# Optimization experiments

Measured on AMD Instinct MI355X. Metric: run time of the kernel, lower is better.

## Reference

```python
import jax, jax.numpy as jnp
import numpy as np

ALPHA = 0.2
NEG_INF = -9e15


def setup_inputs() -> dict:
    key = jax.random.key(0)
    k1, k2, k3, k4 = jax.random.split(key, 4)
    B, N, C_IN, C_OUT, R, H = 8, 1024, 256, 256, 4, 4
    node_feats = jax.random.normal(k1, (B, N, C_IN), dtype=jnp.float32)
    adj_matrix = jax.random.randint(k2, (B, N, N, R), 0, 2, dtype=jnp.int32)
    # xavier_uniform with gain=1.414 for Linear(c_in, c_out) weights
    lim_w = 1.414 * np.sqrt(6.0 / (C_IN + C_OUT))
    W = jax.random.uniform(k3, (R, C_IN, C_OUT), minval=-lim_w, maxval=lim_w, dtype=jnp.float32)
    c_per = C_OUT // H
    lim_a = 1.414 * np.sqrt(6.0 / (H + 2 * c_per))
    a = jax.random.uniform(k4, (R, H, 2 * c_per), minval=-lim_a, maxval=lim_a, dtype=jnp.float32)
    return {"node_feats": node_feats, "adj_matrix": adj_matrix, "W": W, "a": a}


def reference(node_feats, adj_matrix, W, a):
    B, N, _ = node_feats.shape
    R, H = a.shape[0], a.shape[1]
    C = a.shape[2] // 2  # per-head feature dim
    out = jnp.zeros((B, N, H, C), dtype=node_feats.dtype)
    for r in range(R):
        # per-relation projection: [B,N,H,C]
        f = jnp.einsum('bnc,cd->bnd', node_feats, W[r]).reshape(B, N, H, C)
        a_l, a_r = a[r, :, :C], a[r, :, C:]
        # attention logit decomposes: a . [f_i || f_j] = a_l . f_i + a_r . f_j
        li = jnp.einsum('bnhc,hc->bnh', f, a_l)  # source-node term
        lj = jnp.einsum('bnhc,hc->bnh', f, a_r)  # target-node term
        logits = jax.nn.leaky_relu(li[:, :, None, :] + lj[:, None, :, :], ALPHA)  # [B,N,N,H]
        mask = adj_matrix[..., r] != 0  # [B,N,N]
        logits = jnp.where(mask[..., None], logits, NEG_INF)
        probs = jax.nn.softmax(logits, axis=2)
        out = out + jnp.einsum('bijh,bjhc->bihc', probs, f)
    # concat_heads=True
    return out.reshape(B, N, H * C)
```

## Files before the change

### kernel.cpp

```cpp
#include <hip/hip_runtime.h>
#include <math.h>

#define Bsz 8
#define Nn 1024
#define CIN 256
#define COUT 256
#define NR 4
#define NH 4

typedef unsigned short u16;
typedef __attribute__((ext_vector_type(8))) short bf16x8;
typedef __attribute__((ext_vector_type(4))) float f32x4;
typedef __attribute__((ext_vector_type(2))) float f32x2;

#define OFF_LIP (16u << 20)
#define OFF_LJP ((16u << 20) + (512u << 10))
#define OFF_ADJM (17u << 20)
#define OFF_XBF (21u << 20)
#define OFF_WBFT (25u << 20)
#define OFF_WAL ((25u << 20) + (512u << 10))
#define OFF_WAR ((25u << 20) + (528u << 10))
#define OFF_OUTR (26u << 20)

#define LOG2E 1.4426950408889634f

__device__ __forceinline__ short f2bf(float x) {
  union { float f; unsigned u; } v; v.f = x;
  unsigned r = (v.u + 0x7FFFu + ((v.u >> 16) & 1u)) >> 16;
  return (short)r;
}

__device__ __forceinline__ float fast_exp2(float x) {
#if __has_builtin(__builtin_amdgcn_exp2f)
  return __builtin_amdgcn_exp2f(x);
#else
  return exp2f(x);
#endif
}

__device__ __forceinline__ int sbfe1(unsigned v, int bit) {
#if __has_builtin(__builtin_amdgcn_sbfe)
  return __builtin_amdgcn_sbfe((int)v, bit, 1);
#else
  return ((int)(v << (31 - bit))) >> 31;
#endif
}

__device__ __forceinline__ unsigned perm_hi16(unsigned hi, unsigned lo) {
#if __has_builtin(__builtin_amdgcn_perm)
  return __builtin_amdgcn_perm(hi, lo, 0x07060302u);
#else
  return (lo >> 16) | (hi & 0xFFFF0000u);
#endif
}

__device__ __forceinline__ void gl_lds16(const void* g, void* l) {
  __builtin_amdgcn_global_load_lds(
      (const __attribute__((address_space(1))) unsigned int*)(unsigned long long)g,
      (__attribute__((address_space(3))) unsigned int*)(unsigned int)(unsigned long long)l,
      16, 0, 0);
}

__global__ __launch_bounds__(256, 8)
void gatt_pack(const int4* __restrict__ adj4, unsigned long long* __restrict__ adjm) {
  const int t = threadIdx.x;
  const int wid = blockIdx.x * 4 + (t >> 6);
  const int lane = t & 63;
  const int jw = wid & 15;
  const int i = (wid >> 4) & 1023;
  const int b = wid >> 14;
  const int j = jw * 64 + lane;
  const int4 av = adj4[(size_t)(b * Nn + i) * Nn + j];
  const unsigned long long b0 = __ballot(av.x != 0);
  const unsigned long long b1 = __ballot(av.y != 0);
  const unsigned long long b2 = __ballot(av.z != 0);
  const unsigned long long b3 = __ballot(av.w != 0);
  if (lane < 4) {
    unsigned long long v = (lane == 0) ? b0 : (lane == 1) ? b1 : (lane == 2) ? b2 : b3;
    adjm[((size_t)((b * Nn + i) * NR + lane)) * 16 + jw] = v;
  }
}

__global__ __launch_bounds__(256, 4)
void gatt_prep(const float* __restrict__ W, const float* __restrict__ a,
               u16* __restrict__ WbfT, float* __restrict__ wa_l,
               float* __restrict__ wa_r) {
  const int t = threadIdx.x;
  if (blockIdx.x < 32) {
    const int r = blockIdx.x >> 3, kc = blockIdx.x & 7;
    u16 pk[32];
#pragma unroll 8
    for (int kk = 0; kk < 32; ++kk)
      pk[kk] = (u16)f2bf(W[(size_t)r * 65536 + (size_t)(kc * 32 + kk) * COUT + t]);
    u16* dst = WbfT + (size_t)r * 65536 + (size_t)t * CIN + kc * 32;
#pragma unroll
    for (int q = 0; q < 4; ++q) *(int4*)(dst + q * 8) = *(int4*)(pk + q * 8);
  } else {
    const int cb = blockIdx.x - 32;
    const int r = cb >> 2, h = cb & 3;
    float sl = 0.f, sr = 0.f;
    const float* Wp = W + (size_t)r * 65536 + (size_t)t * COUT + h * 64;
    const float* ap = a + r * 512 + h * 128;
#pragma unroll 8
    for (int c = 0; c < 64; ++c) {
      const float wv = Wp[c];
      sl = fmaf(wv, ap[c], sl);
      sr = fmaf(wv, ap[64 + c], sr);
    }
    wa_l[(size_t)cb * CIN + t] = sl;
    wa_r[(size_t)cb * CIN + t] = sr;
  }
}

__global__ __launch_bounds__(256, 4)
void gatt_logitx(const float* __restrict__ X, const float4* __restrict__ wal4,
                 const float4* __restrict__ war4, float* __restrict__ Lip,
                 float* __restrict__ Ljp, u16* __restrict__ Xbf) {
  __shared__ float Xs[16 * 260];
  const int t = threadIdx.x;
  const int row0 = blockIdx.x * 16;
  {
    const int il = t >> 4, kq = t & 15;
    const float4* xp = (const float4*)(X + (size_t)(row0 + il) * CIN + kq * 16);
    float4 v[4];
    u16 pk[16];
#pragma unroll
    for (int u = 0; u < 4; ++u) {
      v[u] = xp[u];
      pk[u * 4 + 0] = (u16)f2bf(v[u].x);
      pk[u * 4 + 1] = (u16)f2bf(v[u].y);
      pk[u * 4 + 2] = (u16)f2bf(v[u].z);
      pk[u * 4 + 3] = (u16)f2bf(v[u].w);
    }
    float4* dst = (float4*)(Xs + il * 260 + kq * 16);
#pragma unroll
    for (int u = 0; u < 4; ++u) dst[u] = v[u];
    u16* xb = Xbf + (size_t)(row0 + il) * CIN + kq * 16;
    *(int4*)xb = *(int4*)pk;
    *(int4*)(xb + 8) = *(int4*)(pk + 8);
  }
  __syncthreads();
  const int rl = t >> 4, combo = t & 15;
  float li = 0.f, lj = 0.f;
#pragma unroll 8
  for (int k4 = 0; k4 < 64; ++k4) {
    const float4 x4 = *(const float4*)(Xs + rl * 260 + k4 * 4);
    const float4 wl = wal4[combo * 64 + k4];
    const float4 wr = war4[combo * 64 + k4];
    li += x4.x * wl.x + x4.y * wl.y + x4.z * wl.z + x4.w * wl.w;
    lj += x4.x * wr.x + x4.y * wr.y + x4.z * wr.z + x4.w * wr.w;
  }
  const int g = row0 + rl, b = g >> 10, n = g & 1023;
  const size_t idx = ((size_t)(combo * Bsz + b)) * Nn + n;
  Lip[idx] = li * LOG2E;
  Ljp[idx] = lj * LOG2E;
}

__global__ __launch_bounds__(256)
void gatt_fgemm(const u16* __restrict__ Xbf, const u16* __restrict__ WbfT,
                u16* __restrict__ fTf) {
  __shared__ u16 lds_w[8192];
  __shared__ u16 lds_x[2048];
  const int t = threadIdx.x;
  const int r = blockIdx.x & 3, b = (blockIdx.x >> 2) & 7, ntl = blockIdx.x >> 5;
  const int n0 = ntl * 64;
  const int g0 = b * Nn + n0;
  const int lane = t & 63, w = t >> 6;
  const int m = lane & 15, quad = lane >> 4;
  const int cw = w * 64;
  const int xq = quad ^ (m & 3);

  const u16* Wsrc = WbfT + (size_t)r * 65536;
  f32x4 acc[4][4];
#pragma unroll
  for (int ct = 0; ct < 4; ++ct)
#pragma unroll
    for (int nt = 0; nt < 4; ++nt) acc[ct][nt] = (f32x4){0.f, 0.f, 0.f, 0.f};

  for (int kc = 0; kc < 8; ++kc) {
    __syncthreads();
#pragma unroll
    for (int q = 0; q < 4; ++q) {
      const int s = q * 256 + t;
      const int c = s >> 2, ks = (s & 3) ^ (c & 3);
      gl_lds16(Wsrc + (size_t)c * CIN + kc * 32 + ks * 8, lds_w + s * 8);
    }
    {
      const int s = t;
      const int n = s >> 2, ks = (s & 3) ^ (n & 3);
      gl_lds16(Xbf + (size_t)(g0 + n) * CIN + kc * 32 + ks * 8, lds_x + s * 8);
    }
    __syncthreads();

    bf16x8 af[4], bfr[4];
#pragma unroll
    for (int ct = 0; ct < 4; ++ct)
      af[ct] = *(const bf16x8*)(lds_w + (cw + ct * 16 + m) * 32 + xq * 8);
#pragma unroll
    for (int nt = 0; nt < 4; ++nt)
      bfr[nt] = *(const bf16x8*)(lds_x + (nt * 16 + m) * 32 + xq * 8);
#pragma unroll
    for (int ct = 0; ct < 4; ++ct)
#pragma unroll
      for (int nt = 0; nt < 4; ++nt)
        acc[ct][nt] = __builtin_amdgcn_mfma_f32_16x16x32_bf16(af[ct], bfr[nt], acc[ct][nt], 0, 0, 0);
  }

  u16* fragbase = fTf + (size_t)(((r * Bsz + b) * 4 + w) * 128) * 512;
#pragma unroll
  for (int ct = 0; ct < 4; ++ct) {
#pragma unroll
    for (int ntf = 0; ntf < 4; ++ntf) {
      const int j = n0 + ntf * 16 + m;
      const int jb = j >> 5;
      const int qt = ((ntf & 1) << 1) | (m >> 3);
      const int e = m & 7;
      u16* dst = fragbase + (size_t)((jb * 4 + ct) * 512) + (qt * 16 + quad * 4) * 8 + e;
#pragma unroll
      for (int p = 0; p < 4; ++p) dst[p * 8] = (u16)f2bf(acc[ct][ntf][p]);
    }
  }
}

__global__ __launch_bounds__(256, 4)
void gatt_attn(const unsigned long long* __restrict__ adjm,
               const u16* __restrict__ fTf, const float* __restrict__ Lip,
               const float* __restrict__ Ljp, float* __restrict__ outr) {
  __shared__ float ljs[4 * 1024];

  const int t = threadIdx.x;
  const int comb = blockIdx.x & 31;
  const int b = comb >> 2, r = comb & 3;
  const int i0 = (blockIdx.x >> 5) * 32;
  const int h = t >> 6, lane = t & 63;
  const int m = lane & 15, quad = lane >> 4;
  const int qo = quad * 8;

  {
#pragma unroll
    for (int q = 0; q < 4; ++q) {
      const int s = q * 256 + t;
      const int hh = s >> 8, off = s & 255;
      ((float4*)ljs)[hh * 256 + off] =
          ((const float4*)(Ljp + ((size_t)((r * NH + hh) * Bsz + b)) * Nn))[off];
    }
  }
  __syncthreads();

  const float* lipb = Lip + ((size_t)((r * NH + h) * Bsz + b)) * Nn;
  const float li0 = lipb[i0 + m];
  const float li1 = lipb[i0 + 16 + m];
  const unsigned long long* amp0 = adjm + ((size_t)((b * Nn + i0 + m) * NR + r)) * 16;
  const unsigned long long* amp1 = adjm + ((size_t)((b * Nn + i0 + 16 + m) * NR + r)) * 16;
  const bf16x8* fp = (const bf16x8*)fTf + (size_t)(((r * Bsz + b) * 4 + h)) * 8192;
  const float* ljh = ljs + h * Nn;

  bf16x8 ones;
#pragma unroll
  for (int e = 0; e < 8; ++e) ones[e] = (short)0x3F80;

  f32x4 acc[2][4], den[2];
#pragma unroll
  for (int iw = 0; iw < 2; ++iw) {
    den[iw] = (f32x4){0.f, 0.f, 0.f, 0.f};
#pragma unroll
    for (int nt = 0; nt < 4; ++nt) acc[iw][nt] = (f32x4){0.f, 0.f, 0.f, 0.f};
  }

  for (int jq = 0; jq < 16; ++jq) {
    const uint2 mw0 = *(const uint2*)(amp0 + jq);
    const uint2 mw1 = *(const uint2*)(amp1 + jq);
#pragma unroll
    for (int half = 0; half < 2; ++half) {
      const int jb = jq * 2 + half;
      const unsigned w0 = half ? mw0.y : mw0.x;
      const unsigned w1 = half ? mw1.y : mw1.x;
      const f32x2* lj2p = (const f32x2*)(ljh + jb * 32 + qo);
      bf16x8 bfr[4];
#pragma unroll
      for (int nt = 0; nt < 4; ++nt) bfr[nt] = fp[(jb * 4 + nt) * 64 + lane];
#pragma unroll
      for (int iw = 0; iw < 2; ++iw) {
        const float liv = iw ? li1 : li0;
        const unsigned mb = (iw ? w1 : w0) >> qo;
        const f32x2 li2 = {liv, liv};
        unsigned afu[4];
#pragma unroll
        for (int pr = 0; pr < 4; ++pr) {
          const f32x2 s2 = li2 + lj2p[pr];
          const f32x2 s02 = s2 * 0.2f;
          const float t0 = fmaxf(s2.x, s02.x);
          const float t1 = fmaxf(s2.y, s02.y);
          const unsigned e0 =
              __float_as_uint(fast_exp2(t0)) & (unsigned)sbfe1(mb, 2 * pr);
          const unsigned e1 =
              __float_as_uint(fast_exp2(t1)) & (unsigned)sbfe1(mb, 2 * pr + 1);
          afu[pr] = perm_hi16(e1, e0);
        }
        union { unsigned u[4]; bf16x8 v; } af;
        af.u[0] = afu[0]; af.u[1] = afu[1]; af.u[2] = afu[2]; af.u[3] = afu[3];
        den[iw] = __builtin_amdgcn_mfma_f32_16x16x32_bf16(af.v, ones, den[iw], 0, 0, 0);
#pragma unroll
        for (int nt = 0; nt < 4; ++nt)
          acc[iw][nt] = __builtin_amdgcn_mfma_f32_16x16x32_bf16(af.v, bfr[nt], acc[iw][nt], 0, 0, 0);
      }
    }
  }

#pragma unroll
  for (int iw = 0; iw < 2; ++iw) {
#pragma unroll
    for (int p = 0; p < 4; ++p) {
      const float inv = __builtin_amdgcn_rcpf(den[iw][p]);
      const int i = i0 + iw * 16 + quad * 4 + p;
      float* op = outr + (((size_t)(r * Bsz + b) * Nn) + i) * COUT + h * 64 + m;
#pragma unroll
      for (int nt = 0; nt < 4; ++nt) op[nt * 16] = acc[iw][nt][p] * inv;
    }
  }
}

__global__ __launch_bounds__(256, 8)
void gatt_reduce(const float4* __restrict__ outr4, float4* __restrict__ out4) {
  const int idx = blockIdx.x * 256 + threadIdx.x;
  float4 v0 = outr4[idx];
  float4 v1 = outr4[idx + 524288];
  float4 v2 = outr4[idx + 2 * 524288];
  float4 v3 = outr4[idx + 3 * 524288];
  out4[idx] = make_float4(v0.x + v1.x + v2.x + v3.x, v0.y + v1.y + v2.y + v3.y,
                          v0.z + v1.z + v2.z + v3.z, v0.w + v1.w + v2.w + v3.w);
}

extern "C" void kernel_launch(void* const* d_in, const int* in_sizes, int n_in,
                              void* d_out, int out_size, void* d_ws, size_t ws_size,
                              hipStream_t stream) {
  const float* X = (const float*)d_in[0];
  const int4* adj4 = (const int4*)d_in[1];
  const float* W = (const float*)d_in[2];
  const float* a = (const float*)d_in[3];
  float* out = (float*)d_out;

  char* ws = (char*)d_ws;
  u16* fTf = (u16*)ws;
  float* Lip = (float*)(ws + OFF_LIP);
  float* Ljp = (float*)(ws + OFF_LJP);
  unsigned long long* adjm = (unsigned long long*)(ws + OFF_ADJM);
  u16* Xbf = (u16*)(ws + OFF_XBF);
  u16* WbfT = (u16*)(ws + OFF_WBFT);
  float* wa_l = (float*)(ws + OFF_WAL);
  float* wa_r = (float*)(ws + OFF_WAR);
  float* outr = (float*)(ws + OFF_OUTR);

  gatt_pack<<<dim3(32768), dim3(256), 0, stream>>>(adj4, adjm);
  gatt_prep<<<dim3(48), dim3(256), 0, stream>>>(W, a, WbfT, wa_l, wa_r);
  gatt_logitx<<<dim3(512), dim3(256), 0, stream>>>(X, (const float4*)wa_l,
                                                   (const float4*)wa_r, Lip, Ljp, Xbf);
  gatt_fgemm<<<dim3(512), dim3(256), 0, stream>>>(Xbf, WbfT, fTf);
  gatt_attn<<<dim3(1024), dim3(256), 0, stream>>>(adjm, fTf, Lip, Ljp, outr);
  gatt_reduce<<<dim3(2048), dim3(256), 0, stream>>>((const float4*)outr, (float4*)out);
}
```

Measured before the change: 295.2 us.

## Fuse relation reduction into attention kernel via shared-memory accumulation

The attention kernel now uses 1024-thread blocks, so all four relations and four heads of a 32-row tile run in one block. Per-relation outputs are summed in shared memory in turn, with barriers between relations, and written straight to the final output. This removes the 32 MB intermediate buffer round trip and the separate reduce launch. The cost is a 4x smaller grid (256 blocks) with larger blocks, more shared memory (64 KB), and serialized accumulation steps that may cut occupancy and latency hiding.

```diff
diff --git a/kernel.cpp b/kernel.cpp
--- a/kernel.cpp
+++ b/kernel.cpp
@@ -20,7 +20,6 @@
 #define OFF_WBFT (25u << 20)
 #define OFF_WAL ((25u << 20) + (512u << 10))
 #define OFF_WAR ((25u << 20) + (528u << 10))
-#define OFF_OUTR (26u << 20)
 
 #define LOG2E 1.4426950408889634f
 
@@ -222,27 +221,27 @@
   }
 }
 
-__global__ __launch_bounds__(256, 4)
+__global__ __launch_bounds__(1024, 4)
 void gatt_attn(const unsigned long long* __restrict__ adjm,
                const u16* __restrict__ fTf, const float* __restrict__ Lip,
-               const float* __restrict__ Ljp, float* __restrict__ outr) {
-  __shared__ float ljs[4 * 1024];
-
-  const int t = threadIdx.x;
-  const int comb = blockIdx.x & 31;
-  const int b = comb >> 2, r = comb & 3;
-  const int i0 = (blockIdx.x >> 5) * 32;
-  const int h = t >> 6, lane = t & 63;
+               const float* __restrict__ Ljp, float* __restrict__ out) {
+  __shared__ float smem[16384];
+
+  const int t = threadIdx.x;
+  const int b = blockIdx.x & 7;
+  const int i0 = (blockIdx.x >> 3) * 32;
+  const int w = t >> 6, lane = t & 63;
+  const int r = w & 3, h = w >> 2;
   const int m = lane & 15, quad = lane >> 4;
   const int qo = quad * 8;
 
   {
 #pragma unroll
     for (int q = 0; q < 4; ++q) {
-      const int s = q * 256 + t;
-      const int hh = s >> 8, off = s & 255;
-      ((float4*)ljs)[hh * 256 + off] =
-          ((const float4*)(Ljp + ((size_t)((r * NH + hh) * Bsz + b)) * Nn))[off];
+      const int s = q * 1024 + t;
+      const int combo = s >> 8, off = s & 255;
+      ((float4*)smem)[s] =
+          ((const float4*)(Ljp + ((size_t)(combo * Bsz + b)) * Nn))[off];
     }
   }
   __syncthreads();
@@ -253,7 +252,7 @@
   const unsigned long long* amp0 = adjm + ((size_t)((b * Nn + i0 + m) * NR + r)) * 16;
   const unsigned long long* amp1 = adjm + ((size_t)((b * Nn + i0 + 16 + m) * NR + r)) * 16;
   const bf16x8* fp = (const bf16x8*)fTf + (size_t)(((r * Bsz + b) * 4 + h)) * 8192;
-  const float* ljh = ljs + h * Nn;
+  const float* ljh = smem + (r * NH + h) * Nn;
 
   bf16x8 ones;
 #pragma unroll
@@ -307,28 +306,36 @@
     }
   }
 
-#pragma unroll
-  for (int iw = 0; iw < 2; ++iw) {
-#pragma unroll
-    for (int p = 0; p < 4; ++p) {
-      const float inv = __builtin_amdgcn_rcpf(den[iw][p]);
-      const int i = i0 + iw * 16 + quad * 4 + p;
-      float* op = outr + (((size_t)(r * Bsz + b) * Nn) + i) * COUT + h * 64 + m;
-#pragma unroll
-      for (int nt = 0; nt < 4; ++nt) op[nt * 16] = acc[iw][nt][p] * inv;
-    }
-  }
-}
-
-__global__ __launch_bounds__(256, 8)
-void gatt_reduce(const float4* __restrict__ outr4, float4* __restrict__ out4) {
-  const int idx = blockIdx.x * 256 + threadIdx.x;
-  float4 v0 = outr4[idx];
-  float4 v1 = outr4[idx + 524288];
-  float4 v2 = outr4[idx + 2 * 524288];
-  float4 v3 = outr4[idx + 3 * 524288];
-  out4[idx] = make_float4(v0.x + v1.x + v2.x + v3.x, v0.y + v1.y + v2.y + v3.y,
-                          v0.z + v1.z + v2.z + v3.z, v0.w + v1.w + v2.w + v3.w);
+#define OSTRIDE 260
+  __syncthreads();
+#pragma unroll
+  for (int rr = 0; rr < 4; ++rr) {
+    if (r == rr) {
+#pragma unroll
+      for (int iw = 0; iw < 2; ++iw) {
+#pragma unroll
+        for (int p = 0; p < 4; ++p) {
+          const float inv = __builtin_amdgcn_rcpf(den[iw][p]);
+          float* op = smem + (iw * 16 + quad * 4 + p) * OSTRIDE + h * 64 + m;
+#pragma unroll
+          for (int nt = 0; nt < 4; ++nt) {
+            const float v = acc[iw][nt][p] * inv;
+            if (rr == 0) op[nt * 16] = v;
+            else op[nt * 16] += v;
+          }
+        }
+      }
+    }
+    __syncthreads();
+  }
+
+#pragma unroll
+  for (int q = 0; q < 2; ++q) {
+    const int idx = q * 1024 + t;
+    const int row = idx >> 6, c4 = idx & 63;
+    const float4 v = *(const float4*)(smem + row * OSTRIDE + c4 * 4);
+    ((float4*)out)[((size_t)(b * Nn + i0 + row)) * 64 + c4] = v;
+  }
 }
 
 extern "C" void kernel_launch(void* const* d_in, const int* in_sizes, int n_in,
@@ -349,13 +356,11 @@
   u16* WbfT = (u16*)(ws + OFF_WBFT);
   float* wa_l = (float*)(ws + OFF_WAL);
   float* wa_r = (float*)(ws + OFF_WAR);
-  float* outr = (float*)(ws + OFF_OUTR);
 
   gatt_pack<<<dim3(32768), dim3(256), 0, stream>>>(adj4, adjm);
   gatt_prep<<<dim3(48), dim3(256), 0, stream>>>(W, a, WbfT, wa_l, wa_r);
   gatt_logitx<<<dim3(512), dim3(256), 0, stream>>>(X, (const float4*)wa_l,
                                                    (const float4*)wa_r, Lip, Ljp, Xbf);
   gatt_fgemm<<<dim3(512), dim3(256), 0, stream>>>(Xbf, WbfT, fTf);
-  gatt_attn<<<dim3(1024), dim3(256), 0, stream>>>(adjm, fTf, Lip, Ljp, outr);
-  gatt_reduce<<<dim3(2048), dim3(256), 0, stream>>>((const float4*)outr, (float4*)out);
-}
+  gatt_attn<<<dim3(256), dim3(1024), 0, stream>>>(adjm, fTf, Lip, Ljp, out);
+}
```

Result: no change. 291.3 us (-1.3%).
